# Optimization experiments

Hardware: AMD Instinct MI355X
Metric: run time of the kernel (lower is better)

## Reference

```python
import jax, jax.numpy as jnp
import numpy as np

M = 0.4        # margin
H = 0.333      # margin scaler slope
S = 64.0       # logit scale
BN_MEAN = 20.0     # running_mean of norm normalizer (affine=False, eval stats)
BN_VAR = 100.0 * 100.0
BN_EPS = 1e-3


def setup_inputs() -> dict:
    key = jax.random.key(0)
    k1, k2, k3 = jax.random.split(key, 3)
    embs = jax.random.normal(k1, (1024, 512), dtype=jnp.float32)
    weight = jax.random.normal(k2, (100000, 512), dtype=jnp.float32)
    labels = jax.random.randint(k3, (1024,), 0, 100000)
    return {"embs": embs, "weight": weight, "labels": labels}


def reference(embs, weight, labels):
    n = embs.shape[0]
    rows = jnp.arange(n)
    # feature norms and cosine logits
    norms = jnp.linalg.norm(embs, axis=1, keepdims=True)            # [N,1]
    w_norm = weight / jnp.linalg.norm(weight, axis=1, keepdims=True)  # [C,D]
    logits = (embs / norms) @ w_norm.T                               # [N,C]
    # norm-adaptive margin scaler (BatchNorm1d with running stats, affine=False)
    g = (norms[:, 0] - BN_MEAN) / jnp.sqrt(BN_VAR + BN_EPS)
    g = jnp.clip(g * H, -1.0, 1.0)                                   # [N]
    # angular margin at the label position
    theta = jnp.arccos(jnp.clip(logits.astype(jnp.float32), -0.999, 0.999))
    theta = theta.at[rows, labels].add(-M * g)
    logits_m = jnp.cos(jnp.clip(theta, 0.0, jnp.pi))
    # additive margin at the label position
    logits_m = logits_m.at[rows, labels].add(-(1.0 + M) * g)
    # scaled softmax cross-entropy (mean over batch)
    logp = jax.nn.log_softmax(logits_m * S, axis=-1)
    return -jnp.mean(logp[rows, labels])
```

## Files before the change

### kernel.cpp

```cpp
#include <hip/hip_runtime.h>
#include <math.h>

constexpr int N_ROWS = 1024;
constexpr int DDIM   = 512;
constexpr int C_CLS  = 100000;
constexpr int BM = 128, BN = 128, BK = 32;
constexpr int NT = (C_CLS + BN - 1) / BN;
constexpr int KTILES = DDIM / BK;
constexpr float MARG = 0.4f;
constexpr int WPAD = 100352;

typedef __attribute__((ext_vector_type(8))) short bf16x8;
typedef __attribute__((ext_vector_type(4))) float f32x4;
typedef __attribute__((address_space(1))) const void gvoid_t;
typedef __attribute__((address_space(3))) void lvoid_t;

__device__ __forceinline__ unsigned int f2bf(float x) {
    union { float f; unsigned int u; } v; v.f = x;
    return (v.u + 0x7FFFu + ((v.u >> 16) & 1u)) >> 16;
}

__device__ __forceinline__ float wave_sum(float s) {
    #pragma unroll
    for (int m = 1; m < 64; m <<= 1) s += __shfl_xor(s, m, 64);
    return s;
}

__global__ __launch_bounds__(256) void prep_embs(const float* __restrict__ embs,
                                                 float* __restrict__ g,
                                                 unsigned short* __restrict__ ehat) {
    const int row  = blockIdx.x * 4 + (threadIdx.x >> 6);
    const int lane = threadIdx.x & 63;
    const float4* src = (const float4*)(embs + (size_t)row * DDIM + lane * 8);
    const float4 a = src[0], b = src[1];
    float ss = a.x*a.x + a.y*a.y + a.z*a.z + a.w*a.w
             + b.x*b.x + b.y*b.y + b.z*b.z + b.w*b.w;
    ss = wave_sum(ss);
    const float norm = sqrtf(ss);
    const float rn = 1.f / norm;
    if (lane == 0) {
        float gg = (norm - 20.f) / sqrtf(10000.f + 1e-3f) * 0.333f;
        gg = fminf(fmaxf(gg, -1.f), 1.f);
        g[row] = gg;
    }
    uint4 pk;
    pk.x = f2bf(a.x*rn) | (f2bf(a.y*rn) << 16);
    pk.y = f2bf(a.z*rn) | (f2bf(a.w*rn) << 16);
    pk.z = f2bf(b.x*rn) | (f2bf(b.y*rn) << 16);
    pk.w = f2bf(b.z*rn) | (f2bf(b.w*rn) << 16);
    *(uint4*)(ehat + (size_t)row * DDIM + lane * 8) = pk;
}

__global__ __launch_bounds__(256) void prep_what(const float* __restrict__ w,
                                                 unsigned short* __restrict__ what) {
    const int row  = blockIdx.x * 4 + (threadIdx.x >> 6);
    const int lane = threadIdx.x & 63;
    const float4* src = (const float4*)(w + (size_t)row * DDIM + lane * 8);
    const float4 a = src[0], b = src[1];
    float ss = a.x*a.x + a.y*a.y + a.z*a.z + a.w*a.w
             + b.x*b.x + b.y*b.y + b.z*b.z + b.w*b.w;
    ss = wave_sum(ss);
    const float rn = rsqrtf(ss);
    uint4 pk;
    pk.x = f2bf(a.x*rn) | (f2bf(a.y*rn) << 16);
    pk.y = f2bf(a.z*rn) | (f2bf(a.w*rn) << 16);
    pk.z = f2bf(b.x*rn) | (f2bf(b.y*rn) << 16);
    pk.w = f2bf(b.z*rn) | (f2bf(b.w*rn) << 16);
    *(uint4*)(what + (size_t)row * DDIM + lane * 8) = pk;
}

__global__ __launch_bounds__(256) void prep_wnorm(const float* __restrict__ w,
                                                  float* __restrict__ rnormw) {
    const int row  = blockIdx.x * 4 + (threadIdx.x >> 6);
    const int lane = threadIdx.x & 63;
    const float4* src = (const float4*)(w + (size_t)row * DDIM + lane * 8);
    const float4 a = src[0], b = src[1];
    float ss = a.x*a.x + a.y*a.y + a.z*a.z + a.w*a.w
             + b.x*b.x + b.y*b.y + b.z*b.z + b.w*b.w;
    ss = wave_sum(ss);
    if (lane == 0) rnormw[row] = 1.f / sqrtf(ss);
}

template<int PRE>
__global__ __launch_bounds__(256, 2) void gemm_fused(
        const unsigned short* __restrict__ ehat,
        const unsigned short* __restrict__ whatb,
        const float* __restrict__ weight,
        const float* __restrict__ rnormw,
        const int* __restrict__ labels,
        float* __restrict__ psum,
        float* __restrict__ dlab)
{
    __shared__ __align__(16) unsigned short As[BM * BK];
    __shared__ __align__(16) unsigned short Bs[BN * BK];
    __shared__ float redbuf[2][BM];

    const int bid    = blockIdx.x;
    const int tile_c = bid >> 3;
    const int tile_r = bid & 7;
    const int row0   = tile_r * BM;
    const int col0   = tile_c * BN;

    const int tid  = threadIdx.x;
    const int lane = tid & 63;
    const int wv   = tid >> 6;
    const int wr   = wv >> 1;
    const int wc   = wv & 1;

    f32x4 acc[4][4];
    #pragma unroll
    for (int m = 0; m < 4; ++m)
        #pragma unroll
        for (int n = 0; n < 4; ++n) acc[m][n] = f32x4{0.f, 0.f, 0.f, 0.f};

    const int kq    = tid & 7;
    const int brow0 = tid >> 3;
    int   cidx[4];
    float rnv[4];
    if constexpr (!PRE) {
        #pragma unroll
        for (int p = 0; p < 4; ++p) {
            int c = col0 + p * 32 + brow0;
            c = c < C_CLS ? c : C_CLS - 1;
            cidx[p] = c;
            rnv[p]  = rnormw[c];
        }
    }
    const int srow = lane >> 2;
    const int skc  = (lane & 3) * 8;

    for (int kt = 0; kt < KTILES; ++kt) {
        const int kbase = kt * BK;
        if constexpr (PRE) {
            #pragma unroll
            for (int i = 0; i < 2; ++i) {
                const int ra = (i * 4 + wv) * 16;
                const unsigned short* ga = ehat + (size_t)(row0 + ra + srow) * DDIM + kbase + skc;
                __builtin_amdgcn_global_load_lds((gvoid_t*)ga, (lvoid_t*)(As + ra * BK), 16, 0, 0);
                const unsigned short* gb = whatb + (size_t)(col0 + ra + srow) * DDIM + kbase + skc;
                __builtin_amdgcn_global_load_lds((gvoid_t*)gb, (lvoid_t*)(Bs + ra * BK), 16, 0, 0);
            }
        } else {
            #pragma unroll
            for (int call = 0; call < 2; ++call) {
                const int chunk = call * 256 + tid;
                const uint4 d = *(const uint4*)(ehat + (size_t)(row0 + (chunk >> 2)) * DDIM
                                                + kbase + (chunk & 3) * 8);
                *(uint4*)(As + chunk * 8) = d;
            }
            #pragma unroll
            for (int p = 0; p < 4; ++p) {
                const float4 wd = *(const float4*)(weight + (size_t)cidx[p] * DDIM + kbase + kq * 4);
                const float r = rnv[p];
                const unsigned int lo = f2bf(wd.x * r) | (f2bf(wd.y * r) << 16);
                const unsigned int hi = f2bf(wd.z * r) | (f2bf(wd.w * r) << 16);
                *(uint2*)(Bs + (p * 32 + brow0) * BK + kq * 4) = make_uint2(lo, hi);
            }
        }
        __syncthreads();

        bf16x8 af[4], bf[4];
        const int lr  = lane & 15;
        const int lko = (lane >> 4) * 8;
        #pragma unroll
        for (int m = 0; m < 4; ++m)
            af[m] = *(const bf16x8*)(As + (wr * 64 + m * 16 + lr) * BK + lko);
        #pragma unroll
        for (int n = 0; n < 4; ++n)
            bf[n] = *(const bf16x8*)(Bs + (wc * 64 + n * 16 + lr) * BK + lko);
        #pragma unroll
        for (int m = 0; m < 4; ++m)
            #pragma unroll
            for (int n = 0; n < 4; ++n)
                acc[m][n] = __builtin_amdgcn_mfma_f32_16x16x32_bf16(af[m], bf[n], acc[m][n], 0, 0, 0);
        __syncthreads();
    }

    #pragma unroll
    for (int m = 0; m < 4; ++m) {
        #pragma unroll
        for (int j = 0; j < 4; ++j) {
            const int lrow  = wr * 64 + m * 16 + ((lane >> 4) << 2) + j;
            const int r_abs = row0 + lrow;
            const int lab   = labels[r_abs];
            float s = 0.f;
            #pragma unroll
            for (int n = 0; n < 4; ++n) {
                const int c_abs = col0 + wc * 64 + n * 16 + (lane & 15);
                float v = acc[m][n][j];
                v = fminf(fmaxf(v, -0.999f), 0.999f);
                if (c_abs == lab) dlab[r_abs] = v;
                if (c_abs < C_CLS) s += __expf(64.f * v - 64.f);
            }
            #pragma unroll
            for (int msk = 1; msk < 16; msk <<= 1) s += __shfl_xor(s, msk, 64);
            if ((lane & 15) == 0) redbuf[wc][lrow] = s;
        }
    }
    __syncthreads();
    for (int t = tid; t < BM; t += 256)
        psum[(size_t)(row0 + t) * NT + tile_c] = redbuf[0][t] + redbuf[1][t];
}

__global__ __launch_bounds__(256) void reduce_rows(const float* __restrict__ psum,
                                                   const float* __restrict__ dlab,
                                                   const float* __restrict__ g,
                                                   float* __restrict__ losses) {
    const int row  = blockIdx.x * 4 + (threadIdx.x >> 6);
    const int lane = threadIdx.x & 63;
    const float* p = psum + (size_t)row * NT;
    float s = 0.f;
    for (int t = lane; t < NT; t += 64) s += p[t];
    s = wave_sum(s);
    if (lane == 0) {
        const float v  = dlab[row];
        const float gg = g[row];
        float th = acosf(v) - MARG * gg;
        th = fminf(fmaxf(th, 0.f), 3.14159265358979323846f);
        const float vm = cosf(th) - (1.f + MARG) * gg;
        s = s - __expf(64.f * v - 64.f) + __expf(64.f * vm - 64.f);
        losses[row] = 64.f + logf(s) - 64.f * vm;
    }
}

__global__ __launch_bounds__(256) void final_mean(const float* __restrict__ losses,
                                                  float* __restrict__ out) {
    const int tid = threadIdx.x;
    float s = 0.f;
    #pragma unroll
    for (int i = 0; i < 4; ++i) s += losses[tid + i * 256];
    s = wave_sum(s);
    __shared__ float red[4];
    if ((tid & 63) == 0) red[tid >> 6] = s;
    __syncthreads();
    if (tid == 0) out[0] = (red[0] + red[1] + red[2] + red[3]) * (1.f / 1024.f);
}

extern "C" void kernel_launch(void* const* d_in, const int* in_sizes, int n_in,
                              void* d_out, int out_size, void* d_ws, size_t ws_size,
                              hipStream_t stream) {
    const float* embs   = (const float*)d_in[0];
    const float* weight = (const float*)d_in[1];
    const int*   labels = (const int*)d_in[2];
    float* out = (float*)d_out;
    float* ws  = (float*)d_ws;

    const size_t WHAT_F = (size_t)WPAD * DDIM / 2;
    const size_t EHAT_F = (size_t)N_ROWS * DDIM / 2;
    const size_t PSUM_F = (size_t)N_ROWS * NT;
    const size_t NEED_F = WHAT_F + EHAT_F + PSUM_F + 3 * 1024;

    if (ws_size >= NEED_F * sizeof(float)) {
        unsigned short* what = (unsigned short*)ws;
        unsigned short* ehat = (unsigned short*)(ws + WHAT_F);
        float* psum   = ws + WHAT_F + EHAT_F;
        float* gbuf   = psum + PSUM_F;
        float* dlab   = gbuf + 1024;
        float* losses = dlab + 1024;

        prep_embs<<<N_ROWS / 4, 256, 0, stream>>>(embs, gbuf, ehat);
        prep_what<<<C_CLS / 4, 256, 0, stream>>>(weight, what);
        gemm_fused<1><<<NT * 8, 256, 0, stream>>>(ehat, what, weight, nullptr, labels, psum, dlab);
        reduce_rows<<<N_ROWS / 4, 256, 0, stream>>>(psum, dlab, gbuf, losses);
        final_mean<<<1, 256, 0, stream>>>(losses, out);
    } else {
        float* rnormw = ws + 0;
        float* gbuf   = ws + 100352;
        float* dlab   = ws + 101376;
        float* losses = ws + 102400;
        unsigned short* ehat = (unsigned short*)(ws + 103424);
        float* psum   = ws + 103424 + 262144;

        prep_embs <<<N_ROWS / 4, 256, 0, stream>>>(embs, gbuf, ehat);
        prep_wnorm<<<C_CLS / 4, 256, 0, stream>>>(weight, rnormw);
        gemm_fused<0><<<NT * 8, 256, 0, stream>>>(ehat, nullptr, weight, rnormw, labels, psum, dlab);
        reduce_rows<<<N_ROWS / 4, 256, 0, stream>>>(psum, dlab, gbuf, losses);
        final_mean<<<1, 256, 0, stream>>>(losses, out);
    }
}
```

Baseline: 218.6 us.

## Replace fused GEMM with 256x256 double-buffered swizzled-LDS MFMA kernel

New measurement: 222.6 us. About the same (+1.8%).

```diff
diff --git a/kernel.cpp b/kernel.cpp
--- a/kernel.cpp
+++ b/kernel.cpp
@@ -4,11 +4,10 @@
 constexpr int N_ROWS = 1024;
 constexpr int DDIM   = 512;
 constexpr int C_CLS  = 100000;
-constexpr int BM = 128, BN = 128, BK = 32;
-constexpr int NT = (C_CLS + BN - 1) / BN;
-constexpr int KTILES = DDIM / BK;
 constexpr float MARG = 0.4f;
-constexpr int WPAD = 100352;
+constexpr int WPAD   = 100352;
+constexpr int NT2    = 392;
+constexpr int NT_FB  = 782;
 
 typedef __attribute__((ext_vector_type(8))) short bf16x8;
 typedef __attribute__((ext_vector_type(4))) float f32x4;
@@ -81,18 +80,153 @@
     if (lane == 0) rnormw[row] = 1.f / sqrtf(ss);
 }
 
-template<int PRE>
-__global__ __launch_bounds__(256, 2) void gemm_fused(
+__device__ __forceinline__ void stage_slab(const unsigned short* __restrict__ src,
+                                           int grow0, const unsigned short* lds_row0,
+                                           int kbase, int lane) {
+    const int lr  = lane >> 3;
+    const int c16 = (lane & 7) ^ lr;
+    const unsigned short* g = src + (size_t)(grow0 + lr) * DDIM + kbase + c16 * 8;
+    __builtin_amdgcn_global_load_lds((gvoid_t*)g, (lvoid_t*)lds_row0, 16, 0, 0);
+}
+__device__ __forceinline__ bf16x8 frag_ld(const unsigned short* tile, int row, int ks, int lane) {
+    const int c16 = ((ks << 2) + (lane >> 4)) ^ (lane & 7);
+    return *(const bf16x8*)(tile + row * 64 + c16 * 8);
+}
+
+__global__ __launch_bounds__(512, 2) void gemm256(
         const unsigned short* __restrict__ ehat,
-        const unsigned short* __restrict__ whatb,
+        const unsigned short* __restrict__ what,
+        const int* __restrict__ labels,
+        float* __restrict__ psum,
+        float* __restrict__ dlab)
+{
+    __shared__ __align__(16) unsigned short As[2][256 * 64];
+    __shared__ __align__(16) unsigned short Bs[2][256 * 64];
+
+    const int tid  = threadIdx.x;
+    const int lane = tid & 63;
+    const int wv   = tid >> 6;
+    const int wr   = wv >> 2;
+    const int wc   = wv & 3;
+
+    const int nchunk = (int)gridDim.x >> 3;
+    const int wgid   = ((int)blockIdx.x & 7) * nchunk + ((int)blockIdx.x >> 3);
+    const int tile_c = wgid >> 2;
+    const int tile_r = wgid & 3;
+    const int row0   = tile_r * 256;
+    const int col0   = tile_c * 256;
+
+    f32x4 acc[8][4];
+    #pragma unroll
+    for (int m = 0; m < 8; ++m)
+        #pragma unroll
+        for (int n = 0; n < 4; ++n) acc[m][n] = f32x4{0.f, 0.f, 0.f, 0.f};
+
+    #pragma unroll
+    for (int s = 0; s < 8; ++s) {
+        const int base = (s & 3) * 64 + wv * 8;
+        if (s < 4) stage_slab(ehat, row0 + base, &As[0][base * 64], 0, lane);
+        else       stage_slab(what, col0 + base, &Bs[0][base * 64], 0, lane);
+    }
+    asm volatile("s_waitcnt vmcnt(0)" ::: "memory");
+    __builtin_amdgcn_s_barrier();
+
+    for (int h = 0; h < 8; ++h) {
+        const int cur = h & 1;
+        const unsigned short* At = As[cur];
+        const unsigned short* Bt = Bs[cur];
+        const unsigned short* An = As[cur ^ 1];
+        const unsigned short* Bn = Bs[cur ^ 1];
+        const int kn = (h + 1) * 64;
+        const bool do_stage = (h < 7);
+
+        bf16x8 af[4][2], bf[4][2];
+
+        #pragma unroll
+        for (int q = 0; q < 4; ++q) {
+            const int mh = q >> 1, nh = q & 1;
+            if (q == 0 || q == 2) {
+                #pragma unroll
+                for (int m = 0; m < 4; ++m)
+                    #pragma unroll
+                    for (int ks = 0; ks < 2; ++ks)
+                        af[m][ks] = frag_ld(At, wr * 128 + (mh * 4 + m) * 16 + (lane & 15), ks, lane);
+            }
+            if (q == 0 || q == 1) {
+                #pragma unroll
+                for (int n = 0; n < 2; ++n)
+                    #pragma unroll
+                    for (int ks = 0; ks < 2; ++ks)
+                        bf[nh * 2 + n][ks] = frag_ld(Bt, wc * 64 + (nh * 2 + n) * 16 + (lane & 15), ks, lane);
+            }
+            if (do_stage) {
+                #pragma unroll
+                for (int s = 0; s < 8; ++s) {
+                    const bool mine = (q == 0) ? (s < 3) : (q == 1) ? (s >= 3 && s < 6)
+                                    : (q == 2) ? (s >= 6) : false;
+                    if (mine) {
+                        const int base = (s & 3) * 64 + wv * 8;
+                        if (s < 4) stage_slab(ehat, row0 + base, &An[base * 64], kn, lane);
+                        else       stage_slab(what, col0 + base, &Bn[base * 64], kn, lane);
+                    }
+                }
+            }
+            __builtin_amdgcn_s_barrier();
+            asm volatile("s_waitcnt lgkmcnt(0)" ::: "memory");
+            __builtin_amdgcn_s_setprio(1);
+            #pragma unroll
+            for (int m = 0; m < 4; ++m)
+                #pragma unroll
+                for (int n = 0; n < 2; ++n)
+                    #pragma unroll
+                    for (int ks = 0; ks < 2; ++ks)
+                        acc[mh * 4 + m][nh * 2 + n] =
+                            __builtin_amdgcn_mfma_f32_16x16x32_bf16(af[m][ks], bf[nh * 2 + n][ks],
+                                                                    acc[mh * 4 + m][nh * 2 + n], 0, 0, 0);
+            __builtin_amdgcn_s_setprio(0);
+            if (q == 3) asm volatile("s_waitcnt vmcnt(0)" ::: "memory");
+            __builtin_amdgcn_s_barrier();
+        }
+    }
+
+    float* red = (float*)&As[0][0];
+    #pragma unroll
+    for (int m = 0; m < 8; ++m) {
+        #pragma unroll
+        for (int j = 0; j < 4; ++j) {
+            const int lrow  = wr * 128 + m * 16 + ((lane >> 4) << 2) + j;
+            const int r_abs = row0 + lrow;
+            const int lab   = labels[r_abs];
+            float s = 0.f;
+            #pragma unroll
+            for (int n = 0; n < 4; ++n) {
+                const int c_abs = col0 + wc * 64 + n * 16 + (lane & 15);
+                float v = acc[m][n][j];
+                v = fminf(fmaxf(v, -0.999f), 0.999f);
+                if (c_abs == lab) dlab[r_abs] = v;
+                if (c_abs < C_CLS) s += __expf(64.f * v - 64.f);
+            }
+            #pragma unroll
+            for (int msk = 1; msk < 16; msk <<= 1) s += __shfl_xor(s, msk, 64);
+            if ((lane & 15) == 0) red[wc * 256 + lrow] = s;
+        }
+    }
+    __syncthreads();
+    for (int t = tid; t < 256; t += 512)
+        psum[(size_t)(row0 + t) * NT2 + tile_c] = red[t] + red[256 + t] + red[512 + t] + red[768 + t];
+}
+
+__global__ __launch_bounds__(256, 2) void gemm_fused_fb(
+        const unsigned short* __restrict__ ehat,
         const float* __restrict__ weight,
         const float* __restrict__ rnormw,
         const int* __restrict__ labels,
         float* __restrict__ psum,
         float* __restrict__ dlab)
 {
-    __shared__ __align__(16) unsigned short As[BM * BK];
-    __shared__ __align__(16) unsigned short Bs[BN * BK];
+    constexpr int BM = 128, BN = 128, BK = 32;
+    __shared__ __align__(16) unsigned short Asf[BM * BK];
+    __shared__ __align__(16) unsigned short Bsf[BN * BK];
     __shared__ float redbuf[2][BM];
 
     const int bid    = blockIdx.x;
@@ -117,62 +251,46 @@
     const int brow0 = tid >> 3;
     int   cidx[4];
     float rnv[4];
-    if constexpr (!PRE) {
+    #pragma unroll
+    for (int p = 0; p < 4; ++p) {
+        int c = col0 + p * 32 + brow0;
+        c = c < C_CLS ? c : C_CLS - 1;
+        cidx[p] = c;
+        rnv[p]  = rnormw[c];
+    }
+
+    for (int kt = 0; kt < DDIM / BK; ++kt) {
+        const int kbase = kt * BK;
+        #pragma unroll
+        for (int call = 0; call < 2; ++call) {
+            const int chunk = call * 256 + tid;
+            const uint4 d = *(const uint4*)(ehat + (size_t)(row0 + (chunk >> 2)) * DDIM
+                                            + kbase + (chunk & 3) * 8);
+            *(uint4*)(Asf + chunk * 8) = d;
+        }
         #pragma unroll
         for (int p = 0; p < 4; ++p) {
-            int c = col0 + p * 32 + brow0;
-            c = c < C_CLS ? c : C_CLS - 1;
-            cidx[p] = c;
-            rnv[p]  = rnormw[c];
-        }
-    }
-    const int srow = lane >> 2;
-    const int skc  = (lane & 3) * 8;
-
-    for (int kt = 0; kt < KTILES; ++kt) {
-        const int kbase = kt * BK;
-        if constexpr (PRE) {
-            #pragma unroll
-            for (int i = 0; i < 2; ++i) {
-                const int ra = (i * 4 + wv) * 16;
-                const unsigned short* ga = ehat + (size_t)(row0 + ra + srow) * DDIM + kbase + skc;
-                __builtin_amdgcn_global_load_lds((gvoid_t*)ga, (lvoid_t*)(As + ra * BK), 16, 0, 0);
-                const unsigned short* gb = whatb + (size_t)(col0 + ra + srow) * DDIM + kbase + skc;
-                __builtin_amdgcn_global_load_lds((gvoid_t*)gb, (lvoid_t*)(Bs + ra * BK), 16, 0, 0);
-            }
-        } else {
-            #pragma unroll
-            for (int call = 0; call < 2; ++call) {
-                const int chunk = call * 256 + tid;
-                const uint4 d = *(const uint4*)(ehat + (size_t)(row0 + (chunk >> 2)) * DDIM
-                                                + kbase + (chunk & 3) * 8);
-                *(uint4*)(As + chunk * 8) = d;
-            }
-            #pragma unroll
-            for (int p = 0; p < 4; ++p) {
-                const float4 wd = *(const float4*)(weight + (size_t)cidx[p] * DDIM + kbase + kq * 4);
-                const float r = rnv[p];
-                const unsigned int lo = f2bf(wd.x * r) | (f2bf(wd.y * r) << 16);
-                const unsigned int hi = f2bf(wd.z * r) | (f2bf(wd.w * r) << 16);
-                *(uint2*)(Bs + (p * 32 + brow0) * BK + kq * 4) = make_uint2(lo, hi);
-            }
+            const float4 wd = *(const float4*)(weight + (size_t)cidx[p] * DDIM + kbase + kq * 4);
+            const float r = rnv[p];
+            const unsigned int lo = f2bf(wd.x * r) | (f2bf(wd.y * r) << 16);
+            const unsigned int hi = f2bf(wd.z * r) | (f2bf(wd.w * r) << 16);
+            *(uint2*)(Bsf + (p * 32 + brow0) * BK + kq * 4) = make_uint2(lo, hi);
         }
         __syncthreads();
-
-        bf16x8 af[4], bf[4];
+        bf16x8 af[4], bfr[4];
         const int lr  = lane & 15;
         const int lko = (lane >> 4) * 8;
         #pragma unroll
         for (int m = 0; m < 4; ++m)
-            af[m] = *(const bf16x8*)(As + (wr * 64 + m * 16 + lr) * BK + lko);
+            af[m] = *(const bf16x8*)(Asf + (wr * 64 + m * 16 + lr) * BK + lko);
         #pragma unroll
         for (int n = 0; n < 4; ++n)
-            bf[n] = *(const bf16x8*)(Bs + (wc * 64 + n * 16 + lr) * BK + lko);
+            bfr[n] = *(const bf16x8*)(Bsf + (wc * 64 + n * 16 + lr) * BK + lko);
         #pragma unroll
         for (int m = 0; m < 4; ++m)
             #pragma unroll
             for (int n = 0; n < 4; ++n)
-                acc[m][n] = __builtin_amdgcn_mfma_f32_16x16x32_bf16(af[m], bf[n], acc[m][n], 0, 0, 0);
+                acc[m][n] = __builtin_amdgcn_mfma_f32_16x16x32_bf16(af[m], bfr[n], acc[m][n], 0, 0, 0);
         __syncthreads();
     }
 
@@ -199,18 +317,18 @@
     }
     __syncthreads();
     for (int t = tid; t < BM; t += 256)
-        psum[(size_t)(row0 + t) * NT + tile_c] = redbuf[0][t] + redbuf[1][t];
+        psum[(size_t)(row0 + t) * NT_FB + tile_c] = redbuf[0][t] + redbuf[1][t];
 }
 
 __global__ __launch_bounds__(256) void reduce_rows(const float* __restrict__ psum,
                                                    const float* __restrict__ dlab,
                                                    const float* __restrict__ g,
-                                                   float* __restrict__ losses) {
+                                                   float* __restrict__ losses, int nt) {
     const int row  = blockIdx.x * 4 + (threadIdx.x >> 6);
     const int lane = threadIdx.x & 63;
-    const float* p = psum + (size_t)row * NT;
+    const float* p = psum + (size_t)row * nt;
     float s = 0.f;
-    for (int t = lane; t < NT; t += 64) s += p[t];
+    for (int t = lane; t < nt; t += 64) s += p[t];
     s = wave_sum(s);
     if (lane == 0) {
         const float v  = dlab[row];
@@ -247,7 +365,7 @@
 
     const size_t WHAT_F = (size_t)WPAD * DDIM / 2;
     const size_t EHAT_F = (size_t)N_ROWS * DDIM / 2;
-    const size_t PSUM_F = (size_t)N_ROWS * NT;
+    const size_t PSUM_F = (size_t)N_ROWS * NT2;
     const size_t NEED_F = WHAT_F + EHAT_F + PSUM_F + 3 * 1024;
 
     if (ws_size >= NEED_F * sizeof(float)) {
@@ -260,8 +378,8 @@
 
         prep_embs<<<N_ROWS / 4, 256, 0, stream>>>(embs, gbuf, ehat);
         prep_what<<<C_CLS / 4, 256, 0, stream>>>(weight, what);
-        gemm_fused<1><<<NT * 8, 256, 0, stream>>>(ehat, what, weight, nullptr, labels, psum, dlab);
-        reduce_rows<<<N_ROWS / 4, 256, 0, stream>>>(psum, dlab, gbuf, losses);
+        gemm256<<<NT2 * 4, 512, 0, stream>>>(ehat, what, labels, psum, dlab);
+        reduce_rows<<<N_ROWS / 4, 256, 0, stream>>>(psum, dlab, gbuf, losses, NT2);
         final_mean<<<1, 256, 0, stream>>>(losses, out);
     } else {
         float* rnormw = ws + 0;
@@ -273,8 +391,8 @@
 
         prep_embs <<<N_ROWS / 4, 256, 0, stream>>>(embs, gbuf, ehat);
         prep_wnorm<<<C_CLS / 4, 256, 0, stream>>>(weight, rnormw);
-        gemm_fused<0><<<NT * 8, 256, 0, stream>>>(ehat, nullptr, weight, rnormw, labels, psum, dlab);
-        reduce_rows<<<N_ROWS / 4, 256, 0, stream>>>(psum, dlab, gbuf, losses);
+        gemm_fused_fb<<<NT_FB * 8, 256, 0, stream>>>(ehat, weight, rnormw, labels, psum, dlab);
+        reduce_rows<<<N_ROWS / 4, 256, 0, stream>>>(psum, dlab, gbuf, losses, NT_FB);
         final_mean<<<1, 256, 0, stream>>>(losses, out);
     }
 }
```
